# Performance work log

Hardware: AMD Instinct MI355X
Metric: run time of the kernel (lower is better)

Reference implementation:

```python
import jax, jax.numpy as jnp
import numpy as np

EPS = 1e-12  # F.normalize default eps


def setup_inputs() -> dict:
    key = jax.random.key(0)
    k1, k2, k3, k4 = jax.random.split(key, 4)
    b, c, h, w = 4, 64, 256, 256
    n_class, n = 19, 20
    nc1 = n_class + 1
    content = jax.random.normal(k1, (b, c, h, w), dtype=jnp.float32)
    seg = jax.random.randint(k2, (b, h, w), 0, n_class, dtype=jnp.int32)
    # xavier-normal-ish init for memory params
    key_mem = jax.random.normal(k3, (nc1, c, n), dtype=jnp.float32) * np.sqrt(2.0 / (c + n))
    val_mem = jax.random.normal(k4, (nc1, n, c), dtype=jnp.float32) * np.sqrt(2.0 / (n + c))
    return {"content": content, "seg": seg, "key_mem": key_mem, "val_mem": val_mem}


def reference(content, seg, key_mem, val_mem):
    # content: [b,c,h,w]; seg: [b,h,w] int; key_mem: [K,c,n]; val_mem: [K,n,c], K=n_class+1
    b, c, h, w = content.shape
    K, _, n = key_mem.shape
    p = h * w
    # one-hot class routing (seg shifted by +1 as in original)
    onehot = jax.nn.one_hot(seg.reshape(b, p) + 1, K, dtype=content.dtype)  # [b,p,K]
    # L2-normalize content rows (masked rows in the original are either this
    # normalized vector, for the matching class, or exactly zero)
    cn = content.transpose(0, 2, 3, 1).reshape(b, p, c)
    cn = cn / jnp.maximum(jnp.linalg.norm(cn, axis=-1, keepdims=True), EPS)
    # L2-normalize keys over channel dim (dim=1 of [K,c,n])
    kn = key_mem / jnp.maximum(jnp.linalg.norm(key_mem, axis=1, keepdims=True), EPS)
    # scores for the matching class; non-matching rows are zero -> softmax = uniform 1/n
    scores = jnp.einsum('bpc,kcn->bkpn', cn, kn)         # [b,K,p,n]
    attn = jax.nn.softmax(scores, axis=-1)
    mask = onehot.transpose(0, 2, 1)[..., None]           # [b,K,p,1]
    weight = jnp.where(mask > 0, attn, 1.0 / n)           # [b,K,p,n]
    # bmm with values, then sum over class dim (fused into the einsum)
    out = jnp.einsum('bkpn,knc->bpc', weight, val_mem)    # [b,p,c]
    return out.reshape(b, h, w, c).transpose(0, 3, 1, 2)  # [b,c,h,w]
```

## Files before the change

### kernel.cpp

```cpp
#include <hip/hip_runtime.h>

typedef _Float16 h2 __attribute__((ext_vector_type(2)));
typedef _Float16 h8 __attribute__((ext_vector_type(8)));
typedef float f4 __attribute__((ext_vector_type(4)));
typedef unsigned int uint32;

#define NVAL 20
#define CDIM 64
#define HW   65536
#define NPIX (4*HW)

#define BLK   1024
#define NWAVE (BLK/64)
#define MAXTILES 35
#define MAXSLOT  (MAXTILES*64)

#define KN_OFF      0
#define KN_KSTRIDE  2560
#define VAL_OFF     (20*KN_KSTRIDE)
#define VAL_KSTRIDE 4096
#define VAL_CSTRIDE 64

#define ROW_STRIDE 144
#define ROWS_BYTES (BLK*ROW_STRIDE)
#define INV_OFF   ROWS_BYTES
#define PERM_OFF  (INV_OFF + BLK*4)
#define TCLS_OFF  (PERM_OFF + MAXSLOT*2)
#define FLAG_OFF  (TCLS_OFF + 144)
#define CNT_OFF   (FLAG_OFF + 144)
#define LDS_TOTAL (CNT_OFF + 24*4 + 16)

static __device__ __forceinline__ h2 bch2(uint32 u) { return __builtin_bit_cast(h2, u); }
static __device__ __forceinline__ uint32 bcu(h2 v) { return __builtin_bit_cast(uint32, v); }
static __device__ __forceinline__ h8 bch8(uint4 u) { return __builtin_bit_cast(h8, u); }
static __device__ __forceinline__ h2 pkrtz(float a, float b) {
    return __builtin_bit_cast(h2, __builtin_amdgcn_cvt_pkrtz(a, b));
}

__global__ void prep_kernel(const float* __restrict__ key,
                            const float* __restrict__ val,
                            unsigned char* __restrict__ ws) {
    int i = blockIdx.x * 256 + threadIdx.x;
    if (i < 20*CDIM) {
        int k = i >> 6, c = i & 63;
        const float* vb = val + k*NVAL*CDIM + c;
        float v[NVAL];
        float s = 0.f;
        #pragma unroll
        for (int j = 0; j < NVAL; j++) { v[j] = vb[j*CDIM]; s += v[j]; }
        float t = 0.f;
        for (int kk = 0; kk < 20; kk++) {
            const float* vb2 = val + kk*NVAL*CDIM + c;
            #pragma unroll
            for (int j = 0; j < NVAL; j++) t += vb2[j*CDIM];
        }
        float rest = (t - s) * (1.0f/NVAL);
        uint32* row = (uint32*)(ws + VAL_OFF + (size_t)k*VAL_KSTRIDE + c*VAL_CSTRIDE);
        #pragma unroll
        for (int jp = 0; jp < 10; jp++) row[jp] = bcu(pkrtz(v[2*jp], v[2*jp+1]));
        row[10] = bcu(pkrtz(rest, 0.f));
        #pragma unroll
        for (int jp = 11; jp < 16; jp++) row[jp] = 0u;
    } else if (i < 20*CDIM + 20*NVAL) {
        int idx = i - 20*CDIM;
        int k = idx / NVAL, j = idx % NVAL;
        const float* kb = key + k*CDIM*NVAL + j;
        float x[CDIM];
        float ssq = 0.f;
        #pragma unroll
        for (int c = 0; c < CDIM; c++) { x[c] = kb[c*NVAL]; ssq = fmaf(x[c], x[c], ssq); }
        float inv = 1.0f / fmaxf(sqrtf(ssq), 1e-12f);
        uint32* row = (uint32*)(ws + KN_OFF + (size_t)k*KN_KSTRIDE + j*128);
        #pragma unroll
        for (int cp = 0; cp < 32; cp++) row[cp] = bcu(pkrtz(x[2*cp]*inv, x[2*cp+1]*inv));
    }
}

static __device__ __forceinline__ int2 scan20(const int* cnt, int cls) {
    int acc = 0, mb = 0;
    #pragma unroll
    for (int k = 1; k <= 20; k++) {
        if (k == cls) mb = acc;
        acc += (cnt[k] + 63) & ~63;
    }
    return make_int2(mb, acc >> 6);
}

__global__ __launch_bounds__(BLK, 4) void main_kernel(
        const float* __restrict__ content, const int* __restrict__ seg,
        const unsigned char* __restrict__ tabs, float* __restrict__ out) {
    extern __shared__ unsigned char lds[];
    float* invA = (float*)(lds + INV_OFF);
    unsigned short* perm = (unsigned short*)(lds + PERM_OFF);
    int* tcls  = (int*)(lds + TCLS_OFF);
    int* flags = (int*)(lds + FLAG_OFF);
    int* cnt   = (int*)(lds + CNT_OFF);

    const int tid  = threadIdx.x;
    const int bid  = (int)((blockIdx.x & 7) * 32 + (blockIdx.x >> 3));
    const int gp0  = bid * BLK;
    const int b    = gp0 >> 16;
    const int pim0 = gp0 & (HW - 1);
    float* obase = out + (size_t)b * CDIM * HW + pim0;

    if (tid < 24) cnt[tid] = 0;
    if (tid < MAXTILES) flags[tid] = 0;
    for (int i = tid; i < MAXSLOT; i += BLK) perm[i] = 0xFFFFu;
    __syncthreads();

    const int cls = seg[gp0 + tid] + 1;
    const int myrank = atomicAdd(&cnt[cls], 1);

    {
        const float* cptr = content + (size_t)b * CDIM * HW + pim0 + tid;
        uint2* myrow = (uint2*)(lds + tid * ROW_STRIDE);
        float ssq = 0.f;
        #pragma unroll
        for (int h = 0; h < 2; h++) {
            float xb[32];
            #pragma unroll
            for (int j = 0; j < 32; j++) xb[j] = cptr[(size_t)(h*32 + j) * HW];
            #pragma unroll
            for (int j = 0; j < 32; j++) ssq = fmaf(xb[j], xb[j], ssq);
            #pragma unroll
            for (int q = 0; q < 8; q++) {
                uint2 o;
                o.x = bcu(pkrtz(xb[4*q+0], xb[4*q+1]));
                o.y = bcu(pkrtz(xb[4*q+2], xb[4*q+3]));
                myrow[h*8 + q] = o;
            }
        }
        invA[tid] = 1.0f / fmaxf(sqrtf(ssq), 1e-12f);
    }
    __syncthreads();

    const int2 s = scan20(cnt, cls);
    const int myslot = s.x + myrank;
    const int mytile = myslot >> 6;
    {
        perm[myslot] = (unsigned short)tid;
        tcls[mytile] = cls;
    }
    __syncthreads();

    const int nt   = s.y;
    const int wave = tid >> 6, lane = tid & 63;
    const int g = lane >> 4, r16 = lane & 15;

    for (int t = wave; t < nt; t += NWAVE) {
        const int u = __builtin_amdgcn_readfirstlane(tcls[t]);

        int rowb[4];
        float invn[4];
        bool mine[4];
        #pragma unroll
        for (int n = 0; n < 4; n++) {
            int v = perm[t*64 + n*16 + r16];
            mine[n] = (v != 0xFFFF);
            int l = mine[n] ? v : 0;
            rowb[n] = l * ROW_STRIDE;
            invn[n] = invA[l];
        }

        const unsigned char* knc = tabs + KN_OFF + (size_t)u * KN_KSTRIDE;
        const unsigned char* vc  = tabs + VAL_OFF + (size_t)u * VAL_KSTRIDE;
        uint4 a_sc[2][2];
        #pragma unroll
        for (int m = 0; m < 2; m++)
            #pragma unroll
            for (int ks = 0; ks < 2; ks++)
                a_sc[m][ks] = *(const uint4*)(knc + (m*16 + r16)*128 + (ks*32 + g*8)*2);
        uint4 apv0 = *(const uint4*)(vc + (0*16 + r16)*VAL_CSTRIDE + g*16);
        uint4 apv1 = *(const uint4*)(vc + (1*16 + r16)*VAL_CSTRIDE + g*16);
        uint4 apv2 = *(const uint4*)(vc + (2*16 + r16)*VAL_CSTRIDE + g*16);
        uint4 apv3 = *(const uint4*)(vc + (3*16 + r16)*VAL_CSTRIDE + g*16);

        uint4 b_sc[4][2];
        #pragma unroll
        for (int n = 0; n < 4; n++)
            #pragma unroll
            for (int ks = 0; ks < 2; ks++)
                b_sc[n][ks] = *(const uint4*)(lds + rowb[n] + (ks*32 + g*8)*2);

        f4 sacc[2][4];
        #pragma unroll
        for (int m = 0; m < 2; m++)
            #pragma unroll
            for (int n = 0; n < 4; n++) sacc[m][n] = (f4){0.f,0.f,0.f,0.f};
        #pragma unroll
        for (int ks = 0; ks < 2; ks++)
            #pragma unroll
            for (int m = 0; m < 2; m++)
                #pragma unroll
                for (int n = 0; n < 4; n++)
                    sacc[m][n] = __builtin_amdgcn_mfma_f32_16x16x32_f16(
                        bch8(a_sc[m][ks]), bch8(b_sc[n][ks]), sacc[m][n], 0, 0, 0);

        uint2 w0[4], w1[4];
        #pragma unroll
        for (int n = 0; n < 4; n++) {
            float e0[4], e1[4];
            #pragma unroll
            for (int r = 0; r < 4; r++) e0[r] = __expf(sacc[0][n][r] * invn[n]);
            float arg1 = (g == 0) ? invn[n] : 0.0f;
            #pragma unroll
            for (int r = 0; r < 4; r++) e1[r] = __expf(sacc[1][n][r] * arg1);
            float sum = e0[0]+e0[1]+e0[2]+e0[3];
            sum += (g == 0) ? (e1[0]+e1[1]+e1[2]+e1[3]) : 0.0f;
            sum += __shfl_xor(sum, 16, 64);
            sum += __shfl_xor(sum, 32, 64);
            float wsc = 1.0f / sum;
            w0[n].x = bcu(pkrtz(e0[0]*wsc, e0[1]*wsc));
            w0[n].y = bcu(pkrtz(e0[2]*wsc, e0[3]*wsc));
            uint2 t1;
            if (g == 0)      { t1.x = bcu(pkrtz(e1[0]*wsc, e1[1]*wsc));
                               t1.y = bcu(pkrtz(e1[2]*wsc, e1[3]*wsc)); }
            else if (g == 1) { t1.x = 0x00003C00u; t1.y = 0u; }
            else             { t1.x = 0u; t1.y = 0u; }
            w1[n] = t1;
        }
        #pragma unroll
        for (int n = 0; n < 4; n++) {
            if (mine[n]) {
                *(uint2*)(lds + rowb[n] + g*8)      = w0[n];
                *(uint2*)(lds + rowb[n] + 32 + g*8) = w1[n];
            }
        }

        uint4 b_pv[4];
        #pragma unroll
        for (int n = 0; n < 4; n++)
            b_pv[n] = *(const uint4*)(lds + rowb[n] + g*16);
        #pragma unroll
        for (int m = 0; m < 4; m++) {
            uint4 a = (m == 0) ? apv0 : (m == 1) ? apv1 : (m == 2) ? apv2 : apv3;
            #pragma unroll
            for (int n = 0; n < 4; n++) {
                f4 o = (f4){0.f,0.f,0.f,0.f};
                o = __builtin_amdgcn_mfma_f32_16x16x32_f16(bch8(a), bch8(b_pv[n]), o, 0, 0, 0);
                uint2 ov; ov.x = bcu(pkrtz(o[0], o[1])); ov.y = bcu(pkrtz(o[2], o[3]));
                if (mine[n])
                    *(uint2*)(lds + rowb[n] + m*32 + g*8) = ov;
            }
        }

        __threadfence_block();
        if (lane == 0)
            __hip_atomic_store(&flags[t], 1, __ATOMIC_RELEASE, __HIP_MEMORY_SCOPE_WORKGROUP);
    }

    while (__hip_atomic_load(&flags[mytile], __ATOMIC_ACQUIRE,
                             __HIP_MEMORY_SCOPE_WORKGROUP) == 0) {
        __builtin_amdgcn_s_sleep(1);
    }
    {
        const uint4* r4 = (const uint4*)(lds + tid * ROW_STRIDE);
        float* op = obase + tid;
        #pragma unroll
        for (int q = 0; q < 8; q++) {
            uint4 v = r4[q];
            h2 x = bch2(v.x), y = bch2(v.y), z = bch2(v.z), w = bch2(v.w);
            op[(size_t)(8*q+0) * HW] = (float)x[0];
            op[(size_t)(8*q+1) * HW] = (float)x[1];
            op[(size_t)(8*q+2) * HW] = (float)y[0];
            op[(size_t)(8*q+3) * HW] = (float)y[1];
            op[(size_t)(8*q+4) * HW] = (float)z[0];
            op[(size_t)(8*q+5) * HW] = (float)z[1];
            op[(size_t)(8*q+6) * HW] = (float)w[0];
            op[(size_t)(8*q+7) * HW] = (float)w[1];
        }
    }
}

extern "C" void kernel_launch(void* const* d_in, const int* in_sizes, int n_in,
                              void* d_out, int out_size, void* d_ws, size_t ws_size,
                              hipStream_t stream) {
    const float* content = (const float*)d_in[0];
    const int*   seg     = (const int*)d_in[1];
    const float* key     = (const float*)d_in[2];
    const float* val     = (const float*)d_in[3];
    float* out = (float*)d_out;
    unsigned char* ws = (unsigned char*)d_ws;

    prep_kernel<<<7, 256, 0, stream>>>(key, val, ws);

    (void)hipFuncSetAttribute((const void*)main_kernel,
                              hipFuncAttributeMaxDynamicSharedMemorySize, LDS_TOTAL);
    main_kernel<<<NPIX/BLK, BLK, LDS_TOTAL, stream>>>(content, seg, ws, out);
}
```

Before: 40.13 us.

## Split block into two independent half-groups with staggered start and wave-group syncs

Each 1024-thread block is divided into two independent 512-thread halves. Each half has its own class histogram, permutation, tile list and completion flags, and synchronises through LDS counter barriers instead of __syncthreads. The second half waits until the first finishes its load phase, so one half's global loads overlap with the other half's MFMA compute. The launch-bounds minimum-blocks hint is dropped, which may change register allocation and occupancy. Padding tiles grow because classes are bucketed per half, and spin-wait syncs add risk.

```diff
diff --git a/kernel.cpp b/kernel.cpp
--- a/kernel.cpp
+++ b/kernel.cpp
@@ -11,9 +11,10 @@
 #define NPIX (4*HW)
 
 #define BLK   1024
-#define NWAVE (BLK/64)
-#define MAXTILES 35
-#define MAXSLOT  (MAXTILES*64)
+#define HALF  512
+#define NW_G  8
+#define MAXT_H 28
+#define MSLOT_H (MAXT_H*64)
 
 #define KN_OFF      0
 #define KN_KSTRIDE  2560
@@ -25,10 +26,11 @@
 #define ROWS_BYTES (BLK*ROW_STRIDE)
 #define INV_OFF   ROWS_BYTES
 #define PERM_OFF  (INV_OFF + BLK*4)
-#define TCLS_OFF  (PERM_OFF + MAXSLOT*2)
-#define FLAG_OFF  (TCLS_OFF + 144)
-#define CNT_OFF   (FLAG_OFF + 144)
-#define LDS_TOTAL (CNT_OFF + 24*4 + 16)
+#define TCLS_OFF  (PERM_OFF + 2*MSLOT_H*2)
+#define FLAG_OFF  (TCLS_OFF + 2*MAXT_H*4)
+#define CNT_OFF   (FLAG_OFF + 2*MAXT_H*4)
+#define CTR_OFF   (CNT_OFF + 2*24*4)
+#define LDS_TOTAL (CTR_OFF + 16)
 
 static __device__ __forceinline__ h2 bch2(uint32 u) { return __builtin_bit_cast(h2, u); }
 static __device__ __forceinline__ uint32 bcu(h2 v) { return __builtin_bit_cast(uint32, v); }
@@ -86,40 +88,65 @@
     return make_int2(mb, acc >> 6);
 }
 
-__global__ __launch_bounds__(BLK, 4) void main_kernel(
+static __device__ __forceinline__ void gsync(int* ctr, int lane) {
+    __threadfence_block();
+    if (lane == 0)
+        __hip_atomic_fetch_add(ctr, 1, __ATOMIC_ACQ_REL, __HIP_MEMORY_SCOPE_WORKGROUP);
+    while (__hip_atomic_load(ctr, __ATOMIC_ACQUIRE, __HIP_MEMORY_SCOPE_WORKGROUP) < NW_G)
+        __builtin_amdgcn_s_sleep(1);
+}
+static __device__ __forceinline__ void gwait(int* ctr) {
+    while (__hip_atomic_load(ctr, __ATOMIC_ACQUIRE, __HIP_MEMORY_SCOPE_WORKGROUP) < NW_G)
+        __builtin_amdgcn_s_sleep(1);
+}
+
+__global__ __launch_bounds__(BLK) void main_kernel(
         const float* __restrict__ content, const int* __restrict__ seg,
         const unsigned char* __restrict__ tabs, float* __restrict__ out) {
     extern __shared__ unsigned char lds[];
     float* invA = (float*)(lds + INV_OFF);
     unsigned short* perm = (unsigned short*)(lds + PERM_OFF);
-    int* tcls  = (int*)(lds + TCLS_OFF);
-    int* flags = (int*)(lds + FLAG_OFF);
-    int* cnt   = (int*)(lds + CNT_OFF);
+    int* tclsA  = (int*)(lds + TCLS_OFF);
+    int* flagsA = (int*)(lds + FLAG_OFF);
+    int* cntA   = (int*)(lds + CNT_OFF);
+    int* ctr    = (int*)(lds + CTR_OFF);
 
     const int tid  = threadIdx.x;
+    const int h    = tid >> 9;
+    const int wave = tid >> 6, lane = tid & 63;
+    const int gw   = wave & 7;
+    const int g = lane >> 4, r16 = lane & 15;
     const int bid  = (int)((blockIdx.x & 7) * 32 + (blockIdx.x >> 3));
     const int gp0  = bid * BLK;
     const int b    = gp0 >> 16;
     const int pim0 = gp0 & (HW - 1);
     float* obase = out + (size_t)b * CDIM * HW + pim0;
 
-    if (tid < 24) cnt[tid] = 0;
-    if (tid < MAXTILES) flags[tid] = 0;
-    for (int i = tid; i < MAXSLOT; i += BLK) perm[i] = 0xFFFFu;
+    unsigned short* permh = perm + h * MSLOT_H;
+    int* tclsh  = tclsA  + h * MAXT_H;
+    int* flagsh = flagsA + h * MAXT_H;
+    int* cnth   = cntA   + h * 24;
+
+    if (tid < 48) cntA[tid] = 0;
+    if (tid < 2*MAXT_H) flagsA[tid] = 0;
+    if (tid < 4) ctr[tid] = 0;
+    for (int i = tid; i < 2*MSLOT_H; i += BLK) perm[i] = 0xFFFFu;
     __syncthreads();
 
+    if (h == 1) gwait(&ctr[0]);
+
     const int cls = seg[gp0 + tid] + 1;
-    const int myrank = atomicAdd(&cnt[cls], 1);
+    const int myrank = atomicAdd(&cnth[cls], 1);
 
     {
         const float* cptr = content + (size_t)b * CDIM * HW + pim0 + tid;
         uint2* myrow = (uint2*)(lds + tid * ROW_STRIDE);
         float ssq = 0.f;
         #pragma unroll
-        for (int h = 0; h < 2; h++) {
+        for (int hh = 0; hh < 2; hh++) {
             float xb[32];
             #pragma unroll
-            for (int j = 0; j < 32; j++) xb[j] = cptr[(size_t)(h*32 + j) * HW];
+            for (int j = 0; j < 32; j++) xb[j] = cptr[(size_t)(hh*32 + j) * HW];
             #pragma unroll
             for (int j = 0; j < 32; j++) ssq = fmaf(xb[j], xb[j], ssq);
             #pragma unroll
@@ -127,37 +154,35 @@
                 uint2 o;
                 o.x = bcu(pkrtz(xb[4*q+0], xb[4*q+1]));
                 o.y = bcu(pkrtz(xb[4*q+2], xb[4*q+3]));
-                myrow[h*8 + q] = o;
+                myrow[hh*8 + q] = o;
             }
         }
         invA[tid] = 1.0f / fmaxf(sqrtf(ssq), 1e-12f);
     }
-    __syncthreads();
-
-    const int2 s = scan20(cnt, cls);
+    gsync(&ctr[h], lane);
+
+    const int2 s = scan20(cnth, cls);
     const int myslot = s.x + myrank;
     const int mytile = myslot >> 6;
     {
-        perm[myslot] = (unsigned short)tid;
-        tcls[mytile] = cls;
-    }
-    __syncthreads();
-
-    const int nt   = s.y;
-    const int wave = tid >> 6, lane = tid & 63;
-    const int g = lane >> 4, r16 = lane & 15;
-
-    for (int t = wave; t < nt; t += NWAVE) {
-        const int u = __builtin_amdgcn_readfirstlane(tcls[t]);
+        permh[myslot] = (unsigned short)tid;
+        tclsh[mytile] = cls;
+    }
+    gsync(&ctr[2 + h], lane);
+
+    const int nt = s.y;
+
+    for (int t = gw; t < nt; t += NW_G) {
+        const int u = __builtin_amdgcn_readfirstlane(tclsh[t]);
 
         int rowb[4];
         float invn[4];
         bool mine[4];
         #pragma unroll
         for (int n = 0; n < 4; n++) {
-            int v = perm[t*64 + n*16 + r16];
+            int v = permh[t*64 + n*16 + r16];
             mine[n] = (v != 0xFFFF);
-            int l = mine[n] ? v : 0;
+            int l = mine[n] ? v : (h * HALF);
             rowb[n] = l * ROW_STRIDE;
             invn[n] = invA[l];
         }
@@ -246,10 +271,10 @@
 
         __threadfence_block();
         if (lane == 0)
-            __hip_atomic_store(&flags[t], 1, __ATOMIC_RELEASE, __HIP_MEMORY_SCOPE_WORKGROUP);
-    }
-
-    while (__hip_atomic_load(&flags[mytile], __ATOMIC_ACQUIRE,
+            __hip_atomic_store(&flagsh[t], 1, __ATOMIC_RELEASE, __HIP_MEMORY_SCOPE_WORKGROUP);
+    }
+
+    while (__hip_atomic_load(&flagsh[mytile], __ATOMIC_ACQUIRE,
                              __HIP_MEMORY_SCOPE_WORKGROUP) == 0) {
         __builtin_amdgcn_s_sleep(1);
     }
```

Result: no change. 40.38 us (+0.6%).

## Vectorize content loads/stores with swizzled LDS layout and compute norms from fp16 rows

Applied to the files above, without the earlier changes.

Each wave now reads four channels with 16-byte vector loads across pixels and writes them into LDS rows at a rotated 8-byte offset per chunk, and the output is written back the same way. The fine-grained per-tile flag spin-wait is replaced by one block barrier before the store phase. The per-pixel inverse norm is no longer computed in fp32 from the global loads; it is recomputed inside the tile loop from the fp16 row data using dot2 and cross-lane shuffles. This targets uncoalesced scalar global traffic and LDS bank conflicts, at the cost of extra ALU work per tile and losing the overlap between early stores and late tiles.

```diff
diff --git a/kernel.cpp b/kernel.cpp
--- a/kernel.cpp
+++ b/kernel.cpp
@@ -11,9 +11,9 @@
 #define NPIX (4*HW)
 
 #define BLK   1024
-#define NWAVE (BLK/64)
+#define NWAVE 16
 #define MAXTILES 35
-#define MAXSLOT  (MAXTILES*64)
+#define MSLOT (MAXTILES*64)
 
 #define KN_OFF      0
 #define KN_KSTRIDE  2560
@@ -23,11 +23,9 @@
 
 #define ROW_STRIDE 144
 #define ROWS_BYTES (BLK*ROW_STRIDE)
-#define INV_OFF   ROWS_BYTES
-#define PERM_OFF  (INV_OFF + BLK*4)
-#define TCLS_OFF  (PERM_OFF + MAXSLOT*2)
-#define FLAG_OFF  (TCLS_OFF + 144)
-#define CNT_OFF   (FLAG_OFF + 144)
+#define PERM_OFF  ROWS_BYTES
+#define TCLS_OFF  (PERM_OFF + MSLOT*2)
+#define CNT_OFF   (TCLS_OFF + MAXTILES*4 + 4)
 #define LDS_TOTAL (CNT_OFF + 24*4 + 16)
 
 static __device__ __forceinline__ h2 bch2(uint32 u) { return __builtin_bit_cast(h2, u); }
@@ -35,6 +33,17 @@
 static __device__ __forceinline__ h8 bch8(uint4 u) { return __builtin_bit_cast(h8, u); }
 static __device__ __forceinline__ h2 pkrtz(float a, float b) {
     return __builtin_bit_cast(h2, __builtin_amdgcn_cvt_pkrtz(a, b));
+}
+static __device__ __forceinline__ float dot2acc(h2 a, h2 b, float acc) {
+#if defined(__has_builtin)
+#if __has_builtin(__builtin_amdgcn_fdot2)
+    return __builtin_amdgcn_fdot2(a, b, acc, false);
+#else
+    return acc + (float)a[0]*(float)b[0] + (float)a[1]*(float)b[1];
+#endif
+#else
+    return acc + (float)a[0]*(float)b[0] + (float)a[1]*(float)b[1];
+#endif
 }
 
 __global__ void prep_kernel(const float* __restrict__ key,
@@ -86,72 +95,71 @@
     return make_int2(mb, acc >> 6);
 }
 
-__global__ __launch_bounds__(BLK, 4) void main_kernel(
+__global__ __launch_bounds__(BLK) void main_kernel(
         const float* __restrict__ content, const int* __restrict__ seg,
         const unsigned char* __restrict__ tabs, float* __restrict__ out) {
     extern __shared__ unsigned char lds[];
-    float* invA = (float*)(lds + INV_OFF);
     unsigned short* perm = (unsigned short*)(lds + PERM_OFF);
-    int* tcls  = (int*)(lds + TCLS_OFF);
-    int* flags = (int*)(lds + FLAG_OFF);
-    int* cnt   = (int*)(lds + CNT_OFF);
+    int* tcls = (int*)(lds + TCLS_OFF);
+    int* cnt  = (int*)(lds + CNT_OFF);
 
     const int tid  = threadIdx.x;
+    const int wave = tid >> 6, lane = tid & 63;
+    const int g = lane >> 4, r16 = lane & 15;
     const int bid  = (int)((blockIdx.x & 7) * 32 + (blockIdx.x >> 3));
     const int gp0  = bid * BLK;
     const int b    = gp0 >> 16;
     const int pim0 = gp0 & (HW - 1);
-    float* obase = out + (size_t)b * CDIM * HW + pim0;
 
     if (tid < 24) cnt[tid] = 0;
-    if (tid < MAXTILES) flags[tid] = 0;
-    for (int i = tid; i < MAXSLOT; i += BLK) perm[i] = 0xFFFFu;
+    for (int i = tid; i < MSLOT; i += BLK) perm[i] = 0xFFFFu;
     __syncthreads();
 
     const int cls = seg[gp0 + tid] + 1;
     const int myrank = atomicAdd(&cnt[cls], 1);
 
     {
-        const float* cptr = content + (size_t)b * CDIM * HW + pim0 + tid;
-        uint2* myrow = (uint2*)(lds + tid * ROW_STRIDE);
-        float ssq = 0.f;
-        #pragma unroll
-        for (int h = 0; h < 2; h++) {
-            float xb[32];
-            #pragma unroll
-            for (int j = 0; j < 32; j++) xb[j] = cptr[(size_t)(h*32 + j) * HW];
-            #pragma unroll
-            for (int j = 0; j < 32; j++) ssq = fmaf(xb[j], xb[j], ssq);
-            #pragma unroll
-            for (int q = 0; q < 8; q++) {
+        const float* cb = content + (size_t)b * CDIM * HW
+                          + (size_t)(4*wave) * HW + pim0 + 4*lane;
+        f4 x0[4], x1[4], x2[4], x3[4];
+        #pragma unroll
+        for (int j = 0; j < 4; j++) x0[j] = *(const f4*)(cb + 0*(size_t)HW + j*256);
+        #pragma unroll
+        for (int j = 0; j < 4; j++) x1[j] = *(const f4*)(cb + 1*(size_t)HW + j*256);
+        #pragma unroll
+        for (int j = 0; j < 4; j++) x2[j] = *(const f4*)(cb + 2*(size_t)HW + j*256);
+        #pragma unroll
+        for (int j = 0; j < 4; j++) x3[j] = *(const f4*)(cb + 3*(size_t)HW + j*256);
+
+        const int woff = 8 * ((wave + lane) & 15);
+        #pragma unroll
+        for (int j = 0; j < 4; j++) {
+            unsigned char* rb = lds + (j*256 + 4*lane) * ROW_STRIDE + woff;
+            #pragma unroll
+            for (int i = 0; i < 4; i++) {
                 uint2 o;
-                o.x = bcu(pkrtz(xb[4*q+0], xb[4*q+1]));
-                o.y = bcu(pkrtz(xb[4*q+2], xb[4*q+3]));
-                myrow[h*8 + q] = o;
-            }
-        }
-        invA[tid] = 1.0f / fmaxf(sqrtf(ssq), 1e-12f);
+                o.x = bcu(pkrtz(x0[j][i], x1[j][i]));
+                o.y = bcu(pkrtz(x2[j][i], x3[j][i]));
+                *(uint2*)(rb + i*ROW_STRIDE) = o;
+            }
+        }
     }
     __syncthreads();
 
     const int2 s = scan20(cnt, cls);
-    const int myslot = s.x + myrank;
-    const int mytile = myslot >> 6;
     {
-        perm[myslot] = (unsigned short)tid;
-        tcls[mytile] = cls;
+        int slot = s.x + myrank;
+        perm[slot] = (unsigned short)tid;
+        tcls[slot >> 6] = cls;
     }
     __syncthreads();
 
-    const int nt   = s.y;
-    const int wave = tid >> 6, lane = tid & 63;
-    const int g = lane >> 4, r16 = lane & 15;
+    const int nt = s.y;
 
     for (int t = wave; t < nt; t += NWAVE) {
         const int u = __builtin_amdgcn_readfirstlane(tcls[t]);
 
-        int rowb[4];
-        float invn[4];
+        int rowb[4], q4[4];
         bool mine[4];
         #pragma unroll
         for (int n = 0; n < 4; n++) {
@@ -159,7 +167,7 @@
             mine[n] = (v != 0xFFFF);
             int l = mine[n] ? v : 0;
             rowb[n] = l * ROW_STRIDE;
-            invn[n] = invA[l];
+            q4[n] = (l >> 2) & 15;
         }
 
         const unsigned char* knc = tabs + KN_OFF + (size_t)u * KN_KSTRIDE;
@@ -176,11 +184,31 @@
         uint4 apv3 = *(const uint4*)(vc + (3*16 + r16)*VAL_CSTRIDE + g*16);
 
         uint4 b_sc[4][2];
-        #pragma unroll
-        for (int n = 0; n < 4; n++)
-            #pragma unroll
-            for (int ks = 0; ks < 2; ks++)
-                b_sc[n][ks] = *(const uint4*)(lds + rowb[n] + (ks*32 + g*8)*2);
+        float invn[4];
+        #pragma unroll
+        for (int n = 0; n < 4; n++) {
+            const unsigned char* rp = lds + rowb[n];
+            #pragma unroll
+            for (int ks = 0; ks < 2; ks++) {
+                int s0 = 8*ks + 2*g;
+                uint2 lo = *(const uint2*)(rp + 8*((s0 + q4[n]) & 15));
+                uint2 hi = *(const uint2*)(rp + 8*((s0 + 1 + q4[n]) & 15));
+                uint4 f; f.x = lo.x; f.y = lo.y; f.z = hi.x; f.w = hi.y;
+                b_sc[n][ks] = f;
+            }
+            float ss = 0.f;
+            #pragma unroll
+            for (int ks = 0; ks < 2; ks++) {
+                uint4 f = b_sc[n][ks];
+                ss = dot2acc(bch2(f.x), bch2(f.x), ss);
+                ss = dot2acc(bch2(f.y), bch2(f.y), ss);
+                ss = dot2acc(bch2(f.z), bch2(f.z), ss);
+                ss = dot2acc(bch2(f.w), bch2(f.w), ss);
+            }
+            ss += __shfl_xor(ss, 16, 64);
+            ss += __shfl_xor(ss, 32, 64);
+            invn[n] = 1.0f / fmaxf(sqrtf(ss), 1e-12f);
+        }
 
         f4 sacc[2][4];
         #pragma unroll
@@ -240,34 +268,32 @@
                 o = __builtin_amdgcn_mfma_f32_16x16x32_f16(bch8(a), bch8(b_pv[n]), o, 0, 0, 0);
                 uint2 ov; ov.x = bcu(pkrtz(o[0], o[1])); ov.y = bcu(pkrtz(o[2], o[3]));
                 if (mine[n])
-                    *(uint2*)(lds + rowb[n] + m*32 + g*8) = ov;
-            }
-        }
-
-        __threadfence_block();
-        if (lane == 0)
-            __hip_atomic_store(&flags[t], 1, __ATOMIC_RELEASE, __HIP_MEMORY_SCOPE_WORKGROUP);
-    }
-
-    while (__hip_atomic_load(&flags[mytile], __ATOMIC_ACQUIRE,
-                             __HIP_MEMORY_SCOPE_WORKGROUP) == 0) {
-        __builtin_amdgcn_s_sleep(1);
-    }
+                    *(uint2*)(lds + rowb[n] + 8*((4*m + g + q4[n]) & 15)) = ov;
+            }
+        }
+    }
+    __syncthreads();
+
     {
-        const uint4* r4 = (const uint4*)(lds + tid * ROW_STRIDE);
-        float* op = obase + tid;
-        #pragma unroll
-        for (int q = 0; q < 8; q++) {
-            uint4 v = r4[q];
-            h2 x = bch2(v.x), y = bch2(v.y), z = bch2(v.z), w = bch2(v.w);
-            op[(size_t)(8*q+0) * HW] = (float)x[0];
-            op[(size_t)(8*q+1) * HW] = (float)x[1];
-            op[(size_t)(8*q+2) * HW] = (float)y[0];
-            op[(size_t)(8*q+3) * HW] = (float)y[1];
-            op[(size_t)(8*q+4) * HW] = (float)z[0];
-            op[(size_t)(8*q+5) * HW] = (float)z[1];
-            op[(size_t)(8*q+6) * HW] = (float)w[0];
-            op[(size_t)(8*q+7) * HW] = (float)w[1];
+        const int woff = 8 * ((wave + lane) & 15);
+        float* ob = out + (size_t)b * CDIM * HW + (size_t)(4*wave) * HW + pim0 + 4*lane;
+        #pragma unroll
+        for (int j = 0; j < 4; j++) {
+            const unsigned char* rb = lds + (j*256 + 4*lane) * ROW_STRIDE + woff;
+            f4 v0, v1, v2, v3;
+            #pragma unroll
+            for (int i = 0; i < 4; i++) {
+                uint2 u = *(const uint2*)(rb + i*ROW_STRIDE);
+                h2 a = bch2(u.x), c = bch2(u.y);
+                v0[i] = (float)a[0];
+                v1[i] = (float)a[1];
+                v2[i] = (float)c[0];
+                v3[i] = (float)c[1];
+            }
+            *(f4*)(ob + 0*(size_t)HW + j*256) = v0;
+            *(f4*)(ob + 1*(size_t)HW + j*256) = v1;
+            *(f4*)(ob + 2*(size_t)HW + j*256) = v2;
+            *(f4*)(ob + 3*(size_t)HW + j*256) = v3;
         }
     }
 }
```

Result: slower. 41.38 us (+3.1%).

## Transpose softmax weights via lane shuffles instead of LDS and raise MFMA priority

Applied to the files above, without the earlier changes.

The softmax weights are now redistributed into the value-MFMA B-operand layout with cross-lane shuffles, replacing the round trip of LDS stores and reloads. The score and value MFMA section is wrapped in s_setprio(1) so waves in the compute phase get issue priority over waves that are loading or storing. The launch-bounds occupancy hint is also dropped, which lets the compiler choose register allocation differently. The shuffles cost extra instructions per tile, and the register pressure may change.

```diff
diff --git a/kernel.cpp b/kernel.cpp
--- a/kernel.cpp
+++ b/kernel.cpp
@@ -11,9 +11,9 @@
 #define NPIX (4*HW)
 
 #define BLK   1024
-#define NWAVE (BLK/64)
+#define NWAVE 16
 #define MAXTILES 35
-#define MAXSLOT  (MAXTILES*64)
+#define MSLOT (MAXTILES*64)
 
 #define KN_OFF      0
 #define KN_KSTRIDE  2560
@@ -25,7 +25,7 @@
 #define ROWS_BYTES (BLK*ROW_STRIDE)
 #define INV_OFF   ROWS_BYTES
 #define PERM_OFF  (INV_OFF + BLK*4)
-#define TCLS_OFF  (PERM_OFF + MAXSLOT*2)
+#define TCLS_OFF  (PERM_OFF + MSLOT*2)
 #define FLAG_OFF  (TCLS_OFF + 144)
 #define CNT_OFF   (FLAG_OFF + 144)
 #define LDS_TOTAL (CNT_OFF + 24*4 + 16)
@@ -86,7 +86,7 @@
     return make_int2(mb, acc >> 6);
 }
 
-__global__ __launch_bounds__(BLK, 4) void main_kernel(
+__global__ __launch_bounds__(BLK) void main_kernel(
         const float* __restrict__ content, const int* __restrict__ seg,
         const unsigned char* __restrict__ tabs, float* __restrict__ out) {
     extern __shared__ unsigned char lds[];
@@ -105,7 +105,7 @@
 
     if (tid < 24) cnt[tid] = 0;
     if (tid < MAXTILES) flags[tid] = 0;
-    for (int i = tid; i < MAXSLOT; i += BLK) perm[i] = 0xFFFFu;
+    for (int i = tid; i < MSLOT; i += BLK) perm[i] = 0xFFFFu;
     __syncthreads();
 
     const int cls = seg[gp0 + tid] + 1;
@@ -182,6 +182,8 @@
             for (int ks = 0; ks < 2; ks++)
                 b_sc[n][ks] = *(const uint4*)(lds + rowb[n] + (ks*32 + g*8)*2);
 
+        __builtin_amdgcn_s_setprio(1);
+
         f4 sacc[2][4];
         #pragma unroll
         for (int m = 0; m < 2; m++)
@@ -196,7 +198,7 @@
                     sacc[m][n] = __builtin_amdgcn_mfma_f32_16x16x32_f16(
                         bch8(a_sc[m][ks]), bch8(b_sc[n][ks]), sacc[m][n], 0, 0, 0);
 
-        uint2 w0[4], w1[4];
+        uint4 bpv[4];
         #pragma unroll
         for (int n = 0; n < 4; n++) {
             float e0[4], e1[4];
@@ -210,39 +212,40 @@
             sum += __shfl_xor(sum, 16, 64);
             sum += __shfl_xor(sum, 32, 64);
             float wsc = 1.0f / sum;
-            w0[n].x = bcu(pkrtz(e0[0]*wsc, e0[1]*wsc));
-            w0[n].y = bcu(pkrtz(e0[2]*wsc, e0[3]*wsc));
-            uint2 t1;
-            if (g == 0)      { t1.x = bcu(pkrtz(e1[0]*wsc, e1[1]*wsc));
-                               t1.y = bcu(pkrtz(e1[2]*wsc, e1[3]*wsc)); }
-            else if (g == 1) { t1.x = 0x00003C00u; t1.y = 0u; }
-            else             { t1.x = 0u; t1.y = 0u; }
-            w1[n] = t1;
-        }
-        #pragma unroll
-        for (int n = 0; n < 4; n++) {
-            if (mine[n]) {
-                *(uint2*)(lds + rowb[n] + g*8)      = w0[n];
-                *(uint2*)(lds + rowb[n] + 32 + g*8) = w1[n];
-            }
-        }
-
-        uint4 b_pv[4];
-        #pragma unroll
-        for (int n = 0; n < 4; n++)
-            b_pv[n] = *(const uint4*)(lds + rowb[n] + g*16);
+            uint32 pk0 = bcu(pkrtz(e0[0]*wsc, e0[1]*wsc));
+            uint32 pk1 = bcu(pkrtz(e0[2]*wsc, e0[3]*wsc));
+            uint32 pk2 = bcu(pkrtz(e1[0]*wsc, e1[1]*wsc));
+            uint32 pk3 = bcu(pkrtz(e1[2]*wsc, e1[3]*wsc));
+            int selA = r16 + ((g == 1) ? 32 : 0);
+            int selB = r16 + ((g == 1) ? 48 : 16);
+            uint32 t0 = (uint32)__shfl((int)pk0, selA, 64);
+            uint32 t1 = (uint32)__shfl((int)pk1, selA, 64);
+            uint32 t2 = (uint32)__shfl((int)pk0, selB, 64);
+            uint32 t3 = (uint32)__shfl((int)pk1, selB, 64);
+            uint32 u0 = (uint32)__shfl((int)pk2, r16, 64);
+            uint32 u1 = (uint32)__shfl((int)pk3, r16, 64);
+            uint4 f;
+            f.x = (g < 2) ? t0 : ((g == 2) ? u0 : 0u);
+            f.y = (g < 2) ? t1 : ((g == 2) ? u1 : 0u);
+            f.z = (g < 2) ? t2 : ((g == 2) ? 0x00003C00u : 0u);
+            f.w = (g < 2) ? t3 : 0u;
+            bpv[n] = f;
+        }
+
         #pragma unroll
         for (int m = 0; m < 4; m++) {
             uint4 a = (m == 0) ? apv0 : (m == 1) ? apv1 : (m == 2) ? apv2 : apv3;
             #pragma unroll
             for (int n = 0; n < 4; n++) {
                 f4 o = (f4){0.f,0.f,0.f,0.f};
-                o = __builtin_amdgcn_mfma_f32_16x16x32_f16(bch8(a), bch8(b_pv[n]), o, 0, 0, 0);
+                o = __builtin_amdgcn_mfma_f32_16x16x32_f16(bch8(a), bch8(bpv[n]), o, 0, 0, 0);
                 uint2 ov; ov.x = bcu(pkrtz(o[0], o[1])); ov.y = bcu(pkrtz(o[2], o[3]));
                 if (mine[n])
                     *(uint2*)(lds + rowb[n] + m*32 + g*8) = ov;
             }
         }
+
+        __builtin_amdgcn_s_setprio(0);
 
         __threadfence_block();
         if (lane == 0)
```

New measurement: 40.09 us (median of 2 runs). Within noise of the previous version (-0.1%).
